# Kernel optimization log

Measured on AMD Instinct MI355X. Metric: run time of the kernel, lower is better.

## Reference

```python
import jax, jax.numpy as jnp
import numpy as np

B, S, V, D, H, L, FF = 2, 1024, 32000, 512, 8, 4, 2048
DK = D // H
WIN, GLOB = 128, 16
EPS = 1e-5


def setup_inputs() -> dict:
    key = jax.random.key(0)
    ks = jax.random.split(key, 12)
    def rn(k, shape, s=0.02):
        return jax.random.normal(k, shape, jnp.float32) * s
    ln2 = jnp.stack([jnp.ones((L, 2, D)), jnp.zeros((L, 2, D))], axis=2)   # [L, 2 norms, (scale,bias), D]
    ln3 = jnp.stack([jnp.ones((L, 3, D)), jnp.zeros((L, 3, D))], axis=2)   # [L, 3 norms, (scale,bias), D]
    fln = jnp.stack([jnp.ones((D,)), jnp.zeros((D,))], axis=0)             # [(scale,bias), D]
    return {
        "src": jax.random.randint(ks[0], (B, S), 0, V),
        "tgt": jax.random.randint(ks[1], (B, S), 0, V),
        "enc_embed": rn(ks[2], (V, D)),
        "dec_embed": rn(ks[3], (V, D)),
        "enc_attn_w": rn(ks[4], (L, 4, D, D)),   # q,k,v,o projections
        "enc_attn_b": jnp.zeros((L, 4, D)),
        "enc_ln": ln2,
        "enc_ffn_w1": rn(ks[5], (L, D, FF)),
        "enc_ffn_b1": jnp.zeros((L, FF)),
        "enc_ffn_w2": rn(ks[6], (L, FF, D)),
        "enc_ffn_b2": jnp.zeros((L, D)),
        "enc_final_ln": fln,
        "dec_attn_w": rn(ks[7], (L, 8, D, D)),   # self q,k,v,o then cross q,k,v,o
        "dec_attn_b": jnp.zeros((L, 8, D)),
        "dec_ln": ln3,
        "dec_ffn_w1": rn(ks[8], (L, D, FF)),
        "dec_ffn_b1": jnp.zeros((L, FF)),
        "dec_ffn_w2": rn(ks[9], (L, FF, D)),
        "dec_ffn_b2": jnp.zeros((L, D)),
        "dec_final_ln": fln,
        "out_w": rn(ks[10], (D, V)),
        "out_b": jnp.zeros((V,)),
    }


def _ln(x, p):
    m = jnp.mean(x, -1, keepdims=True)
    v = jnp.var(x, -1, keepdims=True)
    return p[0] * (x - m) * jax.lax.rsqrt(v + EPS) + p[1]


def _rope(x):
    # x: [B, H, S, DK]; half-split rotary embedding
    half = DK // 2
    pos = jnp.arange(x.shape[2], dtype=jnp.float32)
    inv = 1.0 / (10000.0 ** (jnp.arange(half, dtype=jnp.float32) / half))
    ang = pos[:, None] * inv[None, :]                   # [S, half]
    c, s = jnp.cos(ang), jnp.sin(ang)
    x1, x2 = x[..., :half], x[..., half:]
    return jnp.concatenate([x1 * c - x2 * s, x1 * s + x2 * c], axis=-1)


def _mask(n, causal):
    # local sliding window + global tokens, optional causal
    i = jnp.arange(n)[:, None]
    j = jnp.arange(n)[None, :]
    allowed = jnp.abs(i - j) <= WIN
    allowed = allowed | (i < GLOB) | (j < GLOB)
    if causal:
        allowed = allowed & (j <= i)
    return allowed


def _attn(q_in, k_in, v_in, w, b, causal):
    # w: [4, D, D] (q,k,v,o), b: [4, D]
    def heads(x, idx):
        y = x @ w[idx] + b[idx]
        return y.reshape(x.shape[0], x.shape[1], H, DK).transpose(0, 2, 1, 3)  # [B,H,S,DK]
    Q, K, Vh = heads(q_in, 0), heads(k_in, 1), heads(v_in, 2)
    Q, K = _rope(Q), _rope(K)
    scores = jnp.einsum('bhqd,bhkd->bhqk', Q, K) / np.sqrt(DK).astype(np.float32)
    scores = jnp.where(_mask(q_in.shape[1], causal)[None, None], scores, -1e9)
    A = jax.nn.softmax(scores, axis=-1)
    o = jnp.einsum('bhqk,bhkd->bhqd', A, Vh).transpose(0, 2, 1, 3).reshape(q_in.shape[0], q_in.shape[1], D)
    return o @ w[3] + b[3]


def _ffn(x, w1, b1, w2, b2):
    return jax.nn.gelu(x @ w1 + b1) @ w2 + b2


def _forward(src, tgt, enc_embed, dec_embed, enc_attn_w, enc_attn_b, enc_ln,
             enc_ffn_w1, enc_ffn_b1, enc_ffn_w2, enc_ffn_b2, enc_final_ln,
             dec_attn_w, dec_attn_b, dec_ln, dec_ffn_w1, dec_ffn_b1,
             dec_ffn_w2, dec_ffn_b2, dec_final_ln, out_w, out_b):
    sqrt_d = np.sqrt(D).astype(np.float32)
    # encoder
    x = enc_embed[src] * sqrt_d
    for l in range(L):
        n = _ln(x, enc_ln[l, 0])
        x = x + _attn(n, n, n, enc_attn_w[l], enc_attn_b[l], False)
        n = _ln(x, enc_ln[l, 1])
        x = x + _ffn(n, enc_ffn_w1[l], enc_ffn_b1[l], enc_ffn_w2[l], enc_ffn_b2[l])
    mem = _ln(x, enc_final_ln)
    # decoder
    y = dec_embed[tgt] * sqrt_d
    for l in range(L):
        n = _ln(y, dec_ln[l, 0])
        y = y + _attn(n, n, n, dec_attn_w[l, :4], dec_attn_b[l, :4], True)
        n = _ln(y, dec_ln[l, 1])
        y = y + _attn(n, mem, mem, dec_attn_w[l, 4:], dec_attn_b[l, 4:], False)
        n = _ln(y, dec_ln[l, 2])
        y = y + _ffn(n, dec_ffn_w1[l], dec_ffn_b1[l], dec_ffn_w2[l], dec_ffn_b2[l])
    y = _ln(y, dec_final_ln)
    return y @ out_w + out_b


def reference(src, tgt, enc_embed, dec_embed, enc_attn_w, enc_attn_b, enc_ln,
              enc_ffn_w1, enc_ffn_b1, enc_ffn_w2, enc_ffn_b2, enc_final_ln,
              dec_attn_w, dec_attn_b, dec_ln, dec_ffn_w1, dec_ffn_b1,
              dec_ffn_w2, dec_ffn_b2, dec_final_ln, out_w, out_b):
    return _forward(src, tgt, enc_embed, dec_embed, enc_attn_w, enc_attn_b, enc_ln,
                    enc_ffn_w1, enc_ffn_b1, enc_ffn_w2, enc_ffn_b2, enc_final_ln,
                    dec_attn_w, dec_attn_b, dec_ln, dec_ffn_w1, dec_ffn_b1,
                    dec_ffn_w2, dec_ffn_b2, dec_final_ln, out_w, out_b)
```

## Files before the change

kernel.cpp:

```cpp
#include <hip/hip_runtime.h>
#include <cstdint>
#include <cstddef>

#define S_LEN 1024
#define DM 512
#define NHEAD 8
#define HDIM 64
#define NLAYER 4
#define FFD 2048
#define VOC 32000
#define WINSZ 128
#define GLOBSZ 16

using half8 = __attribute__((ext_vector_type(8))) _Float16;
using f32x4 = __attribute__((ext_vector_type(4))) float;

static __device__ __forceinline__ f32x4 mfma16(half8 a, half8 b, f32x4 c) {
  return __builtin_amdgcn_mfma_f32_16x16x32_f16(a, b, c, 0, 0, 0);
}

typedef __attribute__((address_space(1))) const void gvoid;
typedef __attribute__((address_space(3))) void lvoid;
static __device__ __forceinline__ void gload16(const void* g, void* l) {
  __builtin_amdgcn_global_load_lds((gvoid*)g, (lvoid*)l, 16, 0, 0);
}
template <int N>
static __device__ __forceinline__ void waitv() {
  asm volatile("s_waitcnt vmcnt(%0)" :: "i"(N) : "memory");
}

__global__ __launch_bounds__(256) void transpose2_k(const float* __restrict__ inA,
                                                    const float* __restrict__ inB,
                                                    _Float16* __restrict__ outA,
                                                    _Float16* __restrict__ outB,
                                                    int R, int C, int splitZ)
{
  __shared__ float t[32][33];
  int z = blockIdx.z;
  const float* ip;
  _Float16* op;
  if (z < splitZ) { ip = inA + (size_t)z * R * C; op = outA + (size_t)z * R * C; }
  else { ip = inB + (size_t)(z - splitZ) * R * C; op = outB + (size_t)(z - splitZ) * R * C; }
  int c0 = blockIdx.x * 32, r0 = blockIdx.y * 32;
  int tx = threadIdx.x & 31, ty = threadIdx.x >> 5;
#pragma unroll
  for (int i = 0; i < 32; i += 8)
    t[ty + i][tx] = ip[(size_t)(r0 + ty + i) * C + c0 + tx];
  __syncthreads();
#pragma unroll
  for (int i = 0; i < 32; i += 8)
    op[(size_t)(c0 + ty + i) * R + r0 + tx] = (_Float16)t[tx][ty + i];
}

__global__ __launch_bounds__(256) void embed2_k(const int* __restrict__ src,
                                                const int* __restrict__ tgt,
                                                const float* __restrict__ enc_embed,
                                                const float* __restrict__ dec_embed,
                                                const float* __restrict__ enc_ln0,
                                                const float* __restrict__ dec_ln0,
                                                float* __restrict__ xbuf,
                                                float* __restrict__ ybuf,
                                                _Float16* __restrict__ nbuf,
                                                _Float16* __restrict__ nbuf2)
{
  int which = blockIdx.y;
  const int* ids = which ? tgt : src;
  const float* emb = which ? dec_embed : enc_embed;
  const float* gamma = which ? dec_ln0 : enc_ln0;
  const float* beta = gamma + 512;
  float* xout = which ? ybuf : xbuf;
  _Float16* nout = which ? nbuf2 : nbuf;

  int row = blockIdx.x * 4 + (threadIdx.x >> 6);
  int lane = threadIdx.x & 63;
  const float* er = emb + (size_t)ids[row] * DM + lane * 8;
  float4 v0 = *(const float4*)er;
  float4 v1 = *(const float4*)(er + 4);
  float vals[8] = {v0.x, v0.y, v0.z, v0.w, v1.x, v1.y, v1.z, v1.w};
  float s = 0.f, ss = 0.f;
#pragma unroll
  for (int j = 0; j < 8; ++j) {
    vals[j] *= 22.627416997969522f;
    s += vals[j]; ss += vals[j] * vals[j];
  }
#pragma unroll
  for (int m = 1; m < 64; m <<= 1) { s += __shfl_xor(s, m); ss += __shfl_xor(ss, m); }
  float mean = s * (1.f / 512.f);
  float var = ss * (1.f / 512.f) - mean * mean;
  float rstd = rsqrtf(var + 1e-5f);
  float* xr = xout + (size_t)row * DM + lane * 8;
  _Float16* orow = nout + (size_t)row * DM + lane * 8;
  const float* gp = gamma + lane * 8;
  const float* bp = beta + lane * 8;
#pragma unroll
  for (int j = 0; j < 8; ++j) {
    xr[j] = vals[j];
    orow[j] = (_Float16)(gp[j] * (vals[j] - mean) * rstd + bp[j]);
  }
}

__global__ __launch_bounds__(256) void ln_k(const float* __restrict__ x,
                                            const float* __restrict__ gamma,
                                            const float* __restrict__ beta,
                                            _Float16* __restrict__ outp)
{
  int row = blockIdx.x * 4 + (threadIdx.x >> 6);
  int lane = threadIdx.x & 63;
  const float* xr = x + (size_t)row * DM + lane * 8;
  float4 v0 = *(const float4*)xr;
  float4 v1 = *(const float4*)(xr + 4);
  float vals[8] = {v0.x, v0.y, v0.z, v0.w, v1.x, v1.y, v1.z, v1.w};
  float s = 0.f, ss = 0.f;
#pragma unroll
  for (int j = 0; j < 8; ++j) { s += vals[j]; ss += vals[j] * vals[j]; }
#pragma unroll
  for (int m = 1; m < 64; m <<= 1) { s += __shfl_xor(s, m); ss += __shfl_xor(ss, m); }
  float mean = s * (1.f / 512.f);
  float var = ss * (1.f / 512.f) - mean * mean;
  float rstd = rsqrtf(var + 1e-5f);
  _Float16* orow = outp + (size_t)row * DM + lane * 8;
  const float* gp = gamma + lane * 8;
  const float* bp = beta + lane * 8;
#pragma unroll
  for (int j = 0; j < 8; ++j)
    orow[j] = (_Float16)(gp[j] * (vals[j] - mean) * rstd + bp[j]);
}

template <int BM, int BN, int EPI, int MODE, bool SWZ = false, bool NT = false>
__global__ __launch_bounds__(256) void gemm_k(const _Float16* __restrict__ A,
                                              const _Float16* __restrict__ B,
                                              const float* __restrict__ bias,
                                              const float* __restrict__ resid,
                                              void* __restrict__ Cout,
                                              _Float16* __restrict__ vtout,
                                              int M, int N, int K)
{
  constexpr bool WIDE = (BN >= 64);
  constexpr int WAVE_M = WIDE ? BM / 4 : BM / 2;
  constexpr int WAVE_N = WIDE ? BN : BN / 2;
  constexpr int FMW = WAVE_M / 16;
  constexpr int FNW = WIDE ? BN / 16 : BN / 32;
  constexpr int LPS = BM / 32 + BN / 32;
  static_assert(MODE == 0 || (WIDE && BN == 64), "rope modes need 64-col waves");

  __shared__ __align__(16) _Float16 As[3][BM * 64];
  __shared__ __align__(16) _Float16 Bs[3][BN * 64];
  const int tid = threadIdx.x;
  const int lane = tid & 63, wid = tid >> 6;
  const int g = lane >> 4, ql = lane & 15;

  int bm, bn;
  if constexpr (SWZ) {
    const int gx = gridDim.x;
    const int nwg = gx * gridDim.y;
    const int orig = blockIdx.y * gx + blockIdx.x;
    const int q = nwg >> 3, r = nwg & 7;
    const int xcd = orig & 7, rest = orig >> 3;
    const int id = (xcd < r ? xcd * (q + 1) : r * (q + 1) + (xcd - r) * q) + rest;
    bm = (id % gx) * BM; bn = (id / gx) * BN;
  } else {
    bm = blockIdx.x * BM; bn = blockIdx.y * BN;
  }
  const int wm = WIDE ? wid * WAVE_M : (wid >> 1) * WAVE_M;
  const int wn = WIDE ? 0 : (wid & 1) * WAVE_N;

  const _Float16* Bp;
  if constexpr (MODE == 2) {
    int srcrow0 = ((bn >> 10) * 8 + 5 + ((bn >> 9) & 1)) * 512 + (bn & 511);
    Bp = B + (size_t)srcrow0 * K;
  } else {
    Bp = B + (size_t)bn * K;
  }

  f32x4 acc[FMW][FNW];
#pragma unroll
  for (int a = 0; a < FMW; ++a)
#pragma unroll
    for (int b = 0; b < FNW; ++b) acc[a][b] = f32x4{0.f, 0.f, 0.f, 0.f};

  auto stage = [&](int buf, int kt) {
#pragma unroll
    for (int r2 = 0; r2 < BM / 32; ++r2) {
      int off = r2 * 4096 + tid * 16;
      int row = off >> 7, slot = (off >> 4) & 7;
      gload16(A + (size_t)(bm + row) * K + kt + ((slot ^ (row & 7)) << 3),
              (char*)&As[buf][0] + r2 * 4096 + wid * 1024);
    }
#pragma unroll
    for (int r2 = 0; r2 < BN / 32; ++r2) {
      int off = r2 * 4096 + tid * 16;
      int row = off >> 7, slot = (off >> 4) & 7;
      gload16(Bp + (size_t)row * K + kt + ((slot ^ (row & 7)) << 3),
              (char*)&Bs[buf][0] + r2 * 4096 + wid * 1024);
    }
  };

  auto compute = [&](int cur) {
#pragma unroll
    for (int kk = 0; kk < 2; ++kk) {
      half8 af[FMW], bf[FNW];
#pragma unroll
      for (int a = 0; a < FMW; ++a) {
        int row = wm + a * 16 + ql;
        af[a] = *(const half8*)((const char*)&As[cur][0] + row * 128 + (((kk * 4 + g) ^ (row & 7)) << 4));
      }
#pragma unroll
      for (int b = 0; b < FNW; ++b) {
        int row = wn + b * 16 + ql;
        bf[b] = *(const half8*)((const char*)&Bs[cur][0] + row * 128 + (((kk * 4 + g) ^ (row & 7)) << 4));
      }
#pragma unroll
      for (int a = 0; a < FMW; ++a)
#pragma unroll
        for (int b = 0; b < FNW; ++b) acc[a][b] = mfma16(af[a], bf[b], acc[a][b]);
    }
  };

  const int nk = K >> 6;
  stage(0, 0);
  stage(1, 64);
  for (int t = 0; t < nk; ++t) {
    if (t + 1 < nk) waitv<LPS>(); else waitv<0>();
    __builtin_amdgcn_s_barrier();
    __builtin_amdgcn_sched_barrier(0);
    compute(t % 3);
    if (t + 2 < nk) stage((t + 2) % 3, (t + 2) << 6);
  }

#pragma unroll
  for (int a = 0; a < FMW; ++a) {
    const int row0 = bm + wm + a * 16 + g * 4;
    float v[FNW][4];
#pragma unroll
    for (int b2 = 0; b2 < FNW; ++b2) {
      int col = bn + wn + b2 * 16 + ql;
      float bv;
      if constexpr (MODE == 2) {
        int bcol = ((col >> 10) * 8 + 5 + ((col >> 9) & 1)) * 512 + (col & 511);
        bv = bias[bcol];
      } else {
        bv = bias[col];
      }
#pragma unroll
      for (int r2 = 0; r2 < 4; ++r2) v[b2][r2] = acc[a][b2][r2] + bv;
    }
    if constexpr (MODE != 0) {
      const int seg = bn >> 9;
      bool dorope = (MODE == 3) || (MODE == 1 && seg < 2) ||
                    (MODE == 2 && ((bn >> 9) & 1) == 0);
      if (dorope) {
        const float scale = (MODE == 3 || (MODE == 1 && seg == 0)) ? 0.125f : 1.0f;
#pragma unroll
        for (int b2 = 0; b2 < 2; ++b2) {
          int d = b2 * 16 + ql;
          float inv = __expf(-(float)d * 0.28782313662425574f);
#pragma unroll
          for (int r2 = 0; r2 < 4; ++r2) {
            float sp = (float)((row0 & 1023) + r2);
            float sn, cs; __sincosf(sp * inv, &sn, &cs);
            float x1 = v[b2][r2], x2 = v[b2 + 2][r2];
            v[b2][r2]     = (x1 * cs - x2 * sn) * scale;
            v[b2 + 2][r2] = (x1 * sn + x2 * cs) * scale;
          }
        }
      }
    }
#pragma unroll
    for (int b2 = 0; b2 < FNW; ++b2) {
      int col = bn + wn + b2 * 16 + ql;
      if constexpr (MODE == 1) {
        if (col < 1024) {
#pragma unroll
          for (int r2 = 0; r2 < 4; ++r2)
            ((_Float16*)Cout)[(size_t)(row0 + r2) * 1024 + col] = (_Float16)v[b2][r2];
        } else {
          int rowidx = ((row0 >> 10) << 9) + (col - 1024);
          union { _Float16 h[4]; uint2 u; } pk;
#pragma unroll
          for (int r2 = 0; r2 < 4; ++r2) pk.h[r2] = (_Float16)v[b2][r2];
          *(uint2*)&vtout[((size_t)rowidx << 10) + (row0 & 1023)] = pk.u;
        }
      } else if constexpr (MODE == 2) {
        if ((col & 1023) < 512) {
#pragma unroll
          for (int r2 = 0; r2 < 4; ++r2)
            ((_Float16*)Cout)[(size_t)(row0 + r2) * 2048 + ((col >> 10) << 9) + (col & 511)] = (_Float16)v[b2][r2];
        } else {
          int rowidx = (col & ~1023) + ((row0 >> 10) << 9) + (col & 511);
          union { _Float16 h[4]; uint2 u; } pk;
#pragma unroll
          for (int r2 = 0; r2 < 4; ++r2) pk.h[r2] = (_Float16)v[b2][r2];
          *(uint2*)&vtout[((size_t)rowidx << 10) + (row0 & 1023)] = pk.u;
        }
      } else {
#pragma unroll
        for (int r2 = 0; r2 < 4; ++r2) {
          float x = v[b2][r2];
          if constexpr (EPI == 1) {
            float u = x;
            x = u / (1.f + __expf(-1.5957691216057308f * (u + 0.044715f * u * u * u)));
          }
          if constexpr (EPI == 2) x += resid[(size_t)(row0 + r2) * N + col];
          if constexpr (EPI == 0 || EPI == 1)
            ((_Float16*)Cout)[(size_t)(row0 + r2) * N + col] = (_Float16)x;
          else if constexpr (NT)
            __builtin_nontemporal_store(x, &((float*)Cout)[(size_t)(row0 + r2) * N + col]);
          else
            ((float*)Cout)[(size_t)(row0 + r2) * N + col] = x;
        }
      }
    }
  }
}

template <bool CAUSAL>
__global__ __launch_bounds__(128) void attn_k(const _Float16* __restrict__ qb, int qs, int qoff,
                                              const _Float16* __restrict__ kb, int ks, int koff,
                                              const _Float16* __restrict__ vt,
                                              _Float16* __restrict__ out)
{
  __shared__ _Float16 plds[2][16 * 40];
  const int bh = blockIdx.y, b = bh >> 3, h = bh & 7;
  const int wid = threadIdx.x >> 6, lane = threadIdx.x & 63;
  const int g = lane >> 4, ql = lane & 15;
  const int q0 = blockIdx.x * 32 + wid * 16;
  const size_t rb = (size_t)b * S_LEN;

  half8 qf0, qf1;
  {
    const _Float16* qp = qb + (rb + q0 + ql) * qs + qoff + h * HDIM + g * 8;
    qf0 = *(const half8*)qp;
    qf1 = *(const half8*)(qp + 32);
  }
  float mrun[4] = {-1e30f, -1e30f, -1e30f, -1e30f};
  float srun[4] = {0.f, 0.f, 0.f, 0.f};
  f32x4 oacc[4];
#pragma unroll
  for (int c = 0; c < 4; ++c) oacc[c] = f32x4{0.f, 0.f, 0.f, 0.f};

  const _Float16* vbase = vt + (((size_t)(b * 512 + h * HDIM)) << 10);
  _Float16* pw = plds[wid];

  auto proc = [&](int k0) {
    const _Float16* kp = kb + (rb + k0 + ql) * ks + koff + h * HDIM + g * 8;
    half8 kf00 = *(const half8*)kp;
    half8 kf01 = *(const half8*)(kp + 32);
    half8 kf10 = *(const half8*)(kp + (size_t)16 * ks);
    half8 kf11 = *(const half8*)(kp + (size_t)16 * ks + 32);

    f32x4 s0 = f32x4{0.f, 0.f, 0.f, 0.f};
    f32x4 s1 = f32x4{0.f, 0.f, 0.f, 0.f};
    s0 = mfma16(qf0, kf00, s0); s0 = mfma16(qf1, kf01, s0);
    s1 = mfma16(qf0, kf10, s1); s1 = mfma16(qf1, kf11, s1);

    float p0[4], p1[4];
#pragma unroll
    for (int r = 0; r < 4; ++r) {
      int i = q0 + 4 * g + r;
      int j0 = k0 + ql, j1 = j0 + 16;
      float a0 = s0[r], a1 = s1[r];
      int d0 = i - j0, d1 = i - j1;
      bool ok0 = (d0 <= WINSZ && d0 >= -WINSZ) || (i < GLOBSZ) || (j0 < GLOBSZ);
      bool ok1 = (d1 <= WINSZ && d1 >= -WINSZ) || (i < GLOBSZ) || (j1 < GLOBSZ);
      if (CAUSAL) { ok0 = ok0 && (j0 <= i); ok1 = ok1 && (j1 <= i); }
      a0 = ok0 ? a0 : -1e9f;
      a1 = ok1 ? a1 : -1e9f;
      float mx = fmaxf(a0, a1);
      mx = fmaxf(mx, __shfl_xor(mx, 1));
      mx = fmaxf(mx, __shfl_xor(mx, 2));
      mx = fmaxf(mx, __shfl_xor(mx, 4));
      mx = fmaxf(mx, __shfl_xor(mx, 8));
      float mnew = fmaxf(mrun[r], mx);
      float alpha = __expf(mrun[r] - mnew);
      float e0 = __expf(a0 - mnew), e1 = __expf(a1 - mnew);
      float ps = e0 + e1;
      ps += __shfl_xor(ps, 1);
      ps += __shfl_xor(ps, 2);
      ps += __shfl_xor(ps, 4);
      ps += __shfl_xor(ps, 8);
      srun[r] = srun[r] * alpha + ps;
      mrun[r] = mnew;
#pragma unroll
      for (int c = 0; c < 4; ++c) oacc[c][r] *= alpha;
      p0[r] = e0; p1[r] = e1;
    }
#pragma unroll
    for (int r = 0; r < 4; ++r) {
      pw[(4 * g + r) * 40 + ql] = (_Float16)p0[r];
      pw[(4 * g + r) * 40 + 16 + ql] = (_Float16)p1[r];
    }
    half8 pa = *(const half8*)&pw[ql * 40 + g * 8];
#pragma unroll
    for (int c = 0; c < 4; ++c) {
      half8 vf = *(const half8*)(vbase + (((size_t)(16 * c + ql)) << 10) + k0 + 8 * g);
      oacc[c] = mfma16(pa, vf, oacc[c]);
    }
  };

  const int kend = CAUSAL ? (q0 + 16) : S_LEN;
  int lo = 0, hi = kend;
  if (q0 >= GLOBSZ) {
    lo = (q0 - WINSZ) & ~31;
    if (lo < 0) lo = 0;
    if (!CAUSAL) {
      int h2 = q0 + 16 + WINSZ;
      hi = (h2 < kend) ? h2 : kend;
    }
  }
  if (lo > 0) proc(0);
  for (int k0 = lo; k0 < hi; k0 += 32) proc(k0);

#pragma unroll
  for (int c = 0; c < 4; ++c)
#pragma unroll
    for (int r = 0; r < 4; ++r) {
      float val = oacc[c][r] / srun[r];
      out[(rb + q0 + 4 * g + r) * DM + h * HDIM + 16 * c + ql] = (_Float16)val;
    }
}

extern "C" void kernel_launch(void* const* d_in, const int* in_sizes, int n_in,
                              void* d_out, int out_size, void* d_ws, size_t ws_size,
                              hipStream_t stream)
{
  const int*   src         = (const int*)d_in[0];
  const int*   tgt         = (const int*)d_in[1];
  const float* enc_embed   = (const float*)d_in[2];
  const float* dec_embed   = (const float*)d_in[3];
  const float* enc_attn_w  = (const float*)d_in[4];
  const float* enc_attn_b  = (const float*)d_in[5];
  const float* enc_ln      = (const float*)d_in[6];
  const float* enc_ffn_w1  = (const float*)d_in[7];
  const float* enc_ffn_b1  = (const float*)d_in[8];
  const float* enc_ffn_w2  = (const float*)d_in[9];
  const float* enc_ffn_b2  = (const float*)d_in[10];
  const float* enc_fln     = (const float*)d_in[11];
  const float* dec_attn_w  = (const float*)d_in[12];
  const float* dec_attn_b  = (const float*)d_in[13];
  const float* dec_ln      = (const float*)d_in[14];
  const float* dec_ffn_w1  = (const float*)d_in[15];
  const float* dec_ffn_b1  = (const float*)d_in[16];
  const float* dec_ffn_w2  = (const float*)d_in[17];
  const float* dec_ffn_b2  = (const float*)d_in[18];
  const float* dec_fln     = (const float*)d_in[19];
  const float* out_w       = (const float*)d_in[20];
  const float* out_b       = (const float*)d_in[21];
  float* logits = (float*)d_out;

  char* wsp = (char*)d_ws;
  size_t off = 0;
  auto alloc = [&](size_t bytes) -> void* {
    void* p = wsp + off;
    off += (bytes + 255) & ~(size_t)255;
    return p;
  };
  _Float16* enc_attn_wt = (_Float16*)alloc((size_t)16 * 512 * 512 * 2);
  _Float16* dec_attn_wt = (_Float16*)alloc((size_t)32 * 512 * 512 * 2);
  _Float16* e_ffn1_wt   = (_Float16*)alloc((size_t)4 * 2048 * 512 * 2);
  _Float16* e_ffn2_wt   = (_Float16*)alloc((size_t)4 * 2048 * 512 * 2);
  _Float16* d_ffn1_wt   = (_Float16*)alloc((size_t)4 * 2048 * 512 * 2);
  _Float16* d_ffn2_wt   = (_Float16*)alloc((size_t)4 * 2048 * 512 * 2);
  _Float16* out_wt      = (_Float16*)alloc((size_t)VOC * 512 * 2);
  float*    xbuf        = (float*)alloc((size_t)2048 * 512 * 4);
  float*    ybuf        = (float*)alloc((size_t)2048 * 512 * 4);
  _Float16* nbuf        = (_Float16*)alloc((size_t)2048 * 512 * 2);
  _Float16* nbuf2       = (_Float16*)alloc((size_t)2048 * 512 * 2);
  _Float16* qkvb        = (_Float16*)alloc((size_t)2048 * 1024 * 2);
  _Float16* aob         = (_Float16*)alloc((size_t)2048 * 512 * 2);
  _Float16* hbuf        = (_Float16*)alloc((size_t)2048 * 2048 * 2);
  _Float16* memb        = (_Float16*)alloc((size_t)2048 * 512 * 2);
  _Float16* cqb         = (_Float16*)alloc((size_t)2048 * 512 * 2);
  _Float16* ckvb        = (_Float16*)alloc((size_t)2048 * 2048 * 2);
  _Float16* vts         = (_Float16*)alloc((size_t)2 * 512 * 1024 * 2);
  _Float16* vtc         = (_Float16*)alloc((size_t)8 * 512 * 1024 * 2);

  transpose2_k<<<dim3(16, 16, 48), 256, 0, stream>>>(enc_attn_w, dec_attn_w,
                                                     enc_attn_wt, dec_attn_wt, 512, 512, 16);
  transpose2_k<<<dim3(64, 16, 8), 256, 0, stream>>>(enc_ffn_w1, dec_ffn_w1,
                                                    e_ffn1_wt, d_ffn1_wt, 512, 2048, 4);
  transpose2_k<<<dim3(16, 64, 8), 256, 0, stream>>>(enc_ffn_w2, dec_ffn_w2,
                                                    e_ffn2_wt, d_ffn2_wt, 2048, 512, 4);
  transpose2_k<<<dim3(1000, 16, 1), 256, 0, stream>>>(out_w, out_w, out_wt, out_wt, 512, VOC, 1);

  embed2_k<<<dim3(512, 2), 256, 0, stream>>>(src, tgt, enc_embed, dec_embed,
                                             enc_ln, dec_ln, xbuf, ybuf, nbuf, nbuf2);

  for (int l = 0; l < NLAYER; ++l) {
    const float* g0 = enc_ln + ((size_t)(l * 2 + 0) * 2 + 0) * 512;
    if (l > 0) ln_k<<<512, 256, 0, stream>>>(xbuf, g0, g0 + 512, nbuf);
    gemm_k<64, 64, 0, 1><<<dim3(32, 24), 256, 0, stream>>>(
        nbuf, enc_attn_wt + (size_t)l * 4 * 262144,
        enc_attn_b + (size_t)l * 4 * 512, nullptr, qkvb, vts, 2048, 1536, 512);
    attn_k<false><<<dim3(32, 16), 128, 0, stream>>>(qkvb, 1024, 0, qkvb, 1024, 512, vts, aob);
    gemm_k<64, 32, 2, 0><<<dim3(32, 16), 256, 0, stream>>>(
        aob, enc_attn_wt + (size_t)(l * 4 + 3) * 262144,
        enc_attn_b + (size_t)(l * 4 + 3) * 512, xbuf, xbuf, nullptr, 2048, 512, 512);
    const float* g1 = enc_ln + ((size_t)(l * 2 + 1) * 2 + 0) * 512;
    ln_k<<<512, 256, 0, stream>>>(xbuf, g1, g1 + 512, nbuf);
    gemm_k<64, 64, 1, 0><<<dim3(32, 32), 256, 0, stream>>>(
        nbuf, e_ffn1_wt + (size_t)l * 2048 * 512,
        enc_ffn_b1 + (size_t)l * 2048, nullptr, hbuf, nullptr, 2048, 2048, 512);
    gemm_k<64, 32, 2, 0><<<dim3(32, 16), 256, 0, stream>>>(
        hbuf, e_ffn2_wt + (size_t)l * 512 * 2048,
        enc_ffn_b2 + (size_t)l * 512, xbuf, xbuf, nullptr, 2048, 512, 2048);
  }
  ln_k<<<512, 256, 0, stream>>>(xbuf, enc_fln, enc_fln + 512, memb);

  gemm_k<64, 64, 0, 2><<<dim3(32, 64), 256, 0, stream>>>(
      memb, dec_attn_wt, dec_attn_b, nullptr, ckvb, vtc, 2048, 4096, 512);

  for (int l = 0; l < NLAYER; ++l) {
    const float* g0 = dec_ln + ((size_t)(l * 3 + 0) * 2 + 0) * 512;
    const _Float16* dn = (l == 0) ? nbuf2 : nbuf;
    if (l > 0) ln_k<<<512, 256, 0, stream>>>(ybuf, g0, g0 + 512, nbuf);
    gemm_k<64, 64, 0, 1><<<dim3(32, 24), 256, 0, stream>>>(
        dn, dec_attn_wt + (size_t)l * 8 * 262144,
        dec_attn_b + (size_t)l * 8 * 512, nullptr, qkvb, vts, 2048, 1536, 512);
    attn_k<true><<<dim3(32, 16), 128, 0, stream>>>(qkvb, 1024, 0, qkvb, 1024, 512, vts, aob);
    gemm_k<64, 32, 2, 0><<<dim3(32, 16), 256, 0, stream>>>(
        aob, dec_attn_wt + (size_t)(l * 8 + 3) * 262144,
        dec_attn_b + (size_t)(l * 8 + 3) * 512, ybuf, ybuf, nullptr, 2048, 512, 512);
    const float* g1 = dec_ln + ((size_t)(l * 3 + 1) * 2 + 0) * 512;
    ln_k<<<512, 256, 0, stream>>>(ybuf, g1, g1 + 512, nbuf);
    gemm_k<64, 64, 0, 3><<<dim3(32, 8), 256, 0, stream>>>(
        nbuf, dec_attn_wt + (size_t)(l * 8 + 4) * 262144,
        dec_attn_b + (size_t)(l * 8 + 4) * 512, nullptr, cqb, nullptr, 2048, 512, 512);
    attn_k<false><<<dim3(32, 16), 128, 0, stream>>>(cqb, 512, 0, ckvb, 2048, l * 512,
                                                    vtc + ((size_t)l << 20), aob);
    gemm_k<64, 32, 2, 0><<<dim3(32, 16), 256, 0, stream>>>(
        aob, dec_attn_wt + (size_t)(l * 8 + 7) * 262144,
        dec_attn_b + (size_t)(l * 8 + 7) * 512, ybuf, ybuf, nullptr, 2048, 512, 512);
    const float* g2 = dec_ln + ((size_t)(l * 3 + 2) * 2 + 0) * 512;
    ln_k<<<512, 256, 0, stream>>>(ybuf, g2, g2 + 512, nbuf);
    gemm_k<64, 64, 1, 0><<<dim3(32, 32), 256, 0, stream>>>(
        nbuf, d_ffn1_wt + (size_t)l * 2048 * 512,
        dec_ffn_b1 + (size_t)l * 2048, nullptr, hbuf, nullptr, 2048, 2048, 512);
    gemm_k<64, 32, 2, 0><<<dim3(32, 16), 256, 0, stream>>>(
        hbuf, d_ffn2_wt + (size_t)l * 512 * 2048,
        dec_ffn_b2 + (size_t)l * 512, ybuf, ybuf, nullptr, 2048, 512, 2048);
  }

  ln_k<<<512, 256, 0, stream>>>(ybuf, dec_fln, dec_fln + 512, nbuf);
  gemm_k<128, 64, 3, 0, true, true><<<dim3(16, 500), 256, 0, stream>>>(
      nbuf, out_wt, out_b, nullptr, logits, nullptr, 2048, VOC, 512);
}
```

Baseline: 976.0 us.

## Fuse LayerNorm into the following GEMM prologue with full-K A tile in LDS

Adds a gemmln_k kernel that reads fp32 residual rows, computes LayerNorm per row, and writes the normalized fp16 row for the whole K=512 into LDS. It then streams B tiles double-buffered to do the projection with the existing RoPE, V-transpose and GELU epilogues. All standalone ln_k launches before QKV, cross-Q, cross-KV and FFN1 GEMMs are removed, and embed no longer normalizes. This drops the fp16 round trip and the extra launches, but each column block recomputes LayerNorm for its 64 rows. The 64KB A tile in LDS may also limit occupancy.

```diff
diff --git a/kernel.cpp b/kernel.cpp
--- a/kernel.cpp
+++ b/kernel.cpp
@@ -56,47 +56,23 @@
                                                 const int* __restrict__ tgt,
                                                 const float* __restrict__ enc_embed,
                                                 const float* __restrict__ dec_embed,
-                                                const float* __restrict__ enc_ln0,
-                                                const float* __restrict__ dec_ln0,
                                                 float* __restrict__ xbuf,
-                                                float* __restrict__ ybuf,
-                                                _Float16* __restrict__ nbuf,
-                                                _Float16* __restrict__ nbuf2)
+                                                float* __restrict__ ybuf)
 {
   int which = blockIdx.y;
   const int* ids = which ? tgt : src;
   const float* emb = which ? dec_embed : enc_embed;
-  const float* gamma = which ? dec_ln0 : enc_ln0;
-  const float* beta = gamma + 512;
   float* xout = which ? ybuf : xbuf;
-  _Float16* nout = which ? nbuf2 : nbuf;
 
   int row = blockIdx.x * 4 + (threadIdx.x >> 6);
   int lane = threadIdx.x & 63;
   const float* er = emb + (size_t)ids[row] * DM + lane * 8;
   float4 v0 = *(const float4*)er;
   float4 v1 = *(const float4*)(er + 4);
-  float vals[8] = {v0.x, v0.y, v0.z, v0.w, v1.x, v1.y, v1.z, v1.w};
-  float s = 0.f, ss = 0.f;
-#pragma unroll
-  for (int j = 0; j < 8; ++j) {
-    vals[j] *= 22.627416997969522f;
-    s += vals[j]; ss += vals[j] * vals[j];
-  }
-#pragma unroll
-  for (int m = 1; m < 64; m <<= 1) { s += __shfl_xor(s, m); ss += __shfl_xor(ss, m); }
-  float mean = s * (1.f / 512.f);
-  float var = ss * (1.f / 512.f) - mean * mean;
-  float rstd = rsqrtf(var + 1e-5f);
   float* xr = xout + (size_t)row * DM + lane * 8;
-  _Float16* orow = nout + (size_t)row * DM + lane * 8;
-  const float* gp = gamma + lane * 8;
-  const float* bp = beta + lane * 8;
-#pragma unroll
-  for (int j = 0; j < 8; ++j) {
-    xr[j] = vals[j];
-    orow[j] = (_Float16)(gp[j] * (vals[j] - mean) * rstd + bp[j]);
-  }
+  const float sc = 22.627416997969522f;
+  xr[0] = v0.x * sc; xr[1] = v0.y * sc; xr[2] = v0.z * sc; xr[3] = v0.w * sc;
+  xr[4] = v1.x * sc; xr[5] = v1.y * sc; xr[6] = v1.z * sc; xr[7] = v1.w * sc;
 }
 
 __global__ __launch_bounds__(256) void ln_k(const float* __restrict__ x,
@@ -124,6 +100,191 @@
 #pragma unroll
   for (int j = 0; j < 8; ++j)
     orow[j] = (_Float16)(gp[j] * (vals[j] - mean) * rstd + bp[j]);
+}
+
+template <int EPI, int MODE>
+__global__ __launch_bounds__(256) void gemmln_k(const float* __restrict__ A,
+                                                const _Float16* __restrict__ B,
+                                                const float* __restrict__ gamma,
+                                                const float* __restrict__ beta,
+                                                const float* __restrict__ bias,
+                                                void* __restrict__ Cout,
+                                                _Float16* __restrict__ vtout,
+                                                int N)
+{
+  constexpr int FNW = 4;
+  __shared__ __align__(16) _Float16 As[64 * 512];
+  __shared__ __align__(16) _Float16 Bs[2][64 * 64];
+  const int tid = threadIdx.x;
+  const int lane = tid & 63, wid = tid >> 6;
+  const int g = lane >> 4, ql = lane & 15;
+  const int bm = blockIdx.x * 64, bn = blockIdx.y * 64;
+
+  const _Float16* Bp;
+  if constexpr (MODE == 2) {
+    int srcrow0 = ((bn >> 10) * 8 + 5 + ((bn >> 9) & 1)) * 512 + (bn & 511);
+    Bp = B + (size_t)srcrow0 * 512;
+  } else {
+    Bp = B + (size_t)bn * 512;
+  }
+
+  auto stageB = [&](int buf, int kt) {
+#pragma unroll
+    for (int r2 = 0; r2 < 2; ++r2) {
+      int off = r2 * 4096 + tid * 16;
+      int row = off >> 7, slot = (off >> 4) & 7;
+      gload16(Bp + (size_t)row * 512 + kt + ((slot ^ (row & 7)) << 3),
+              (char*)&Bs[buf][0] + r2 * 4096 + wid * 1024);
+    }
+  };
+
+  stageB(0, 0);
+
+  {
+    const int row = wid * 16 + (lane >> 2);
+    const int chunk = lane & 3;
+    const float* ap = A + (size_t)(bm + row) * 512 + chunk * 128;
+    float s = 0.f, ss = 0.f;
+#pragma unroll
+    for (int j = 0; j < 32; ++j) {
+      float4 v = *(const float4*)(ap + j * 4);
+      s += v.x + v.y + v.z + v.w;
+      ss += v.x * v.x + v.y * v.y + v.z * v.z + v.w * v.w;
+    }
+    s += __shfl_xor(s, 1); ss += __shfl_xor(ss, 1);
+    s += __shfl_xor(s, 2); ss += __shfl_xor(ss, 2);
+    const float mean = s * (1.f / 512.f);
+    const float rstd = rsqrtf(ss * (1.f / 512.f) - mean * mean + 1e-5f);
+    const float* gp = gamma + chunk * 128;
+    const float* bp = beta + chunk * 128;
+    auto nrm = [&](float a, float gg, float bb) {
+      return (_Float16)(gg * (a - mean) * rstd + bb);
+    };
+#pragma unroll
+    for (int j = 0; j < 16; ++j) {
+      float4 a0 = *(const float4*)(ap + j * 8);
+      float4 a1 = *(const float4*)(ap + j * 8 + 4);
+      float4 g0 = *(const float4*)(gp + j * 8);
+      float4 g1 = *(const float4*)(gp + j * 8 + 4);
+      float4 b0 = *(const float4*)(bp + j * 8);
+      float4 b1 = *(const float4*)(bp + j * 8 + 4);
+      union { _Float16 h[8]; uint4 u; } pk;
+      pk.h[0] = nrm(a0.x, g0.x, b0.x); pk.h[1] = nrm(a0.y, g0.y, b0.y);
+      pk.h[2] = nrm(a0.z, g0.z, b0.z); pk.h[3] = nrm(a0.w, g0.w, b0.w);
+      pk.h[4] = nrm(a1.x, g1.x, b1.x); pk.h[5] = nrm(a1.y, g1.y, b1.y);
+      pk.h[6] = nrm(a1.z, g1.z, b1.z); pk.h[7] = nrm(a1.w, g1.w, b1.w);
+      int slot16 = chunk * 16 + j;
+      int seg = slot16 >> 3, sub = slot16 & 7;
+      *(uint4*)((char*)As + row * 1024 + seg * 128 + ((sub ^ (row & 7)) << 4)) = pk.u;
+    }
+  }
+  asm volatile("s_waitcnt lgkmcnt(0)" ::: "memory");
+
+  f32x4 acc[FNW];
+#pragma unroll
+  for (int b = 0; b < FNW; ++b) acc[b] = f32x4{0.f, 0.f, 0.f, 0.f};
+
+  const int arow = wid * 16 + ql;
+  const int abyte_base = arow * 1024;
+
+#pragma unroll
+  for (int t = 0; t < 8; ++t) {
+    __builtin_amdgcn_s_barrier();
+    if (t + 1 < 8) stageB((t + 1) & 1, (t + 1) << 6);
+    if (t + 1 < 8) waitv<2>(); else waitv<0>();
+    __builtin_amdgcn_sched_barrier(0);
+    const int cur = t & 1;
+#pragma unroll
+    for (int kk = 0; kk < 2; ++kk) {
+      half8 af = *(const half8*)((const char*)As + abyte_base + t * 128 +
+                                 (((kk * 4 + g) ^ (arow & 7)) << 4));
+      half8 bf[FNW];
+#pragma unroll
+      for (int b = 0; b < FNW; ++b) {
+        int row = b * 16 + ql;
+        bf[b] = *(const half8*)((const char*)&Bs[cur][0] + row * 128 +
+                                (((kk * 4 + g) ^ (row & 7)) << 4));
+      }
+#pragma unroll
+      for (int b = 0; b < FNW; ++b) acc[b] = mfma16(af, bf[b], acc[b]);
+    }
+  }
+
+  const int row0 = bm + wid * 16 + g * 4;
+  float v[FNW][4];
+#pragma unroll
+  for (int b2 = 0; b2 < FNW; ++b2) {
+    int col = bn + b2 * 16 + ql;
+    float bv;
+    if constexpr (MODE == 2) {
+      int bcol = ((col >> 10) * 8 + 5 + ((col >> 9) & 1)) * 512 + (col & 511);
+      bv = bias[bcol];
+    } else {
+      bv = bias[col];
+    }
+#pragma unroll
+    for (int r2 = 0; r2 < 4; ++r2) v[b2][r2] = acc[b2][r2] + bv;
+  }
+  if constexpr (MODE != 0) {
+    const int seg = bn >> 9;
+    bool dorope = (MODE == 3) || (MODE == 1 && seg < 2) ||
+                  (MODE == 2 && ((bn >> 9) & 1) == 0);
+    if (dorope) {
+      const float scale = (MODE == 3 || (MODE == 1 && seg == 0)) ? 0.125f : 1.0f;
+#pragma unroll
+      for (int b2 = 0; b2 < 2; ++b2) {
+        int d = b2 * 16 + ql;
+        float inv = __expf(-(float)d * 0.28782313662425574f);
+#pragma unroll
+        for (int r2 = 0; r2 < 4; ++r2) {
+          float sp = (float)((row0 & 1023) + r2);
+          float sn, cs; __sincosf(sp * inv, &sn, &cs);
+          float x1 = v[b2][r2], x2 = v[b2 + 2][r2];
+          v[b2][r2]     = (x1 * cs - x2 * sn) * scale;
+          v[b2 + 2][r2] = (x1 * sn + x2 * cs) * scale;
+        }
+      }
+    }
+  }
+#pragma unroll
+  for (int b2 = 0; b2 < FNW; ++b2) {
+    int col = bn + b2 * 16 + ql;
+    if constexpr (MODE == 1) {
+      if (col < 1024) {
+#pragma unroll
+        for (int r2 = 0; r2 < 4; ++r2)
+          ((_Float16*)Cout)[(size_t)(row0 + r2) * 1024 + col] = (_Float16)v[b2][r2];
+      } else {
+        int rowidx = ((row0 >> 10) << 9) + (col - 1024);
+        union { _Float16 h[4]; uint2 u; } pk;
+#pragma unroll
+        for (int r2 = 0; r2 < 4; ++r2) pk.h[r2] = (_Float16)v[b2][r2];
+        *(uint2*)&vtout[((size_t)rowidx << 10) + (row0 & 1023)] = pk.u;
+      }
+    } else if constexpr (MODE == 2) {
+      if ((col & 1023) < 512) {
+#pragma unroll
+        for (int r2 = 0; r2 < 4; ++r2)
+          ((_Float16*)Cout)[(size_t)(row0 + r2) * 2048 + ((col >> 10) << 9) + (col & 511)] = (_Float16)v[b2][r2];
+      } else {
+        int rowidx = (col & ~1023) + ((row0 >> 10) << 9) + (col & 511);
+        union { _Float16 h[4]; uint2 u; } pk;
+#pragma unroll
+        for (int r2 = 0; r2 < 4; ++r2) pk.h[r2] = (_Float16)v[b2][r2];
+        *(uint2*)&vtout[((size_t)rowidx << 10) + (row0 & 1023)] = pk.u;
+      }
+    } else {
+#pragma unroll
+      for (int r2 = 0; r2 < 4; ++r2) {
+        float x = v[b2][r2];
+        if constexpr (EPI == 1) {
+          float u = x;
+          x = u / (1.f + __expf(-1.5957691216057308f * (u + 0.044715f * u * u * u)));
+        }
+        ((_Float16*)Cout)[(size_t)(row0 + r2) * N + col] = (_Float16)x;
+      }
+    }
+  }
 }
 
 template <int BM, int BN, int EPI, int MODE, bool SWZ = false, bool NT = false>
@@ -141,7 +302,6 @@
   constexpr int FMW = WAVE_M / 16;
   constexpr int FNW = WIDE ? BN / 16 : BN / 32;
   constexpr int LPS = BM / 32 + BN / 32;
-  static_assert(MODE == 0 || (WIDE && BN == 64), "rope modes need 64-col waves");
 
   __shared__ __align__(16) _Float16 As[3][BM * 64];
   __shared__ __align__(16) _Float16 Bs[3][BN * 64];
@@ -164,13 +324,7 @@
   const int wm = WIDE ? wid * WAVE_M : (wid >> 1) * WAVE_M;
   const int wn = WIDE ? 0 : (wid & 1) * WAVE_N;
 
-  const _Float16* Bp;
-  if constexpr (MODE == 2) {
-    int srcrow0 = ((bn >> 10) * 8 + 5 + ((bn >> 9) & 1)) * 512 + (bn & 511);
-    Bp = B + (size_t)srcrow0 * K;
-  } else {
-    Bp = B + (size_t)bn * K;
-  }
+  const _Float16* Bp = B + (size_t)bn * K;
 
   f32x4 acc[FMW][FNW];
 #pragma unroll
@@ -230,84 +384,24 @@
 #pragma unroll
   for (int a = 0; a < FMW; ++a) {
     const int row0 = bm + wm + a * 16 + g * 4;
-    float v[FNW][4];
 #pragma unroll
     for (int b2 = 0; b2 < FNW; ++b2) {
       int col = bn + wn + b2 * 16 + ql;
-      float bv;
-      if constexpr (MODE == 2) {
-        int bcol = ((col >> 10) * 8 + 5 + ((col >> 9) & 1)) * 512 + (col & 511);
-        bv = bias[bcol];
-      } else {
-        bv = bias[col];
-      }
-#pragma unroll
-      for (int r2 = 0; r2 < 4; ++r2) v[b2][r2] = acc[a][b2][r2] + bv;
-    }
-    if constexpr (MODE != 0) {
-      const int seg = bn >> 9;
-      bool dorope = (MODE == 3) || (MODE == 1 && seg < 2) ||
-                    (MODE == 2 && ((bn >> 9) & 1) == 0);
-      if (dorope) {
-        const float scale = (MODE == 3 || (MODE == 1 && seg == 0)) ? 0.125f : 1.0f;
-#pragma unroll
-        for (int b2 = 0; b2 < 2; ++b2) {
-          int d = b2 * 16 + ql;
-          float inv = __expf(-(float)d * 0.28782313662425574f);
-#pragma unroll
-          for (int r2 = 0; r2 < 4; ++r2) {
-            float sp = (float)((row0 & 1023) + r2);
-            float sn, cs; __sincosf(sp * inv, &sn, &cs);
-            float x1 = v[b2][r2], x2 = v[b2 + 2][r2];
-            v[b2][r2]     = (x1 * cs - x2 * sn) * scale;
-            v[b2 + 2][r2] = (x1 * sn + x2 * cs) * scale;
-          }
+      float bv = bias[col];
+#pragma unroll
+      for (int r2 = 0; r2 < 4; ++r2) {
+        float x = acc[a][b2][r2] + bv;
+        if constexpr (EPI == 1) {
+          float u = x;
+          x = u / (1.f + __expf(-1.5957691216057308f * (u + 0.044715f * u * u * u)));
         }
-      }
-    }
-#pragma unroll
-    for (int b2 = 0; b2 < FNW; ++b2) {
-      int col = bn + wn + b2 * 16 + ql;
-      if constexpr (MODE == 1) {
-        if (col < 1024) {
-#pragma unroll
-          for (int r2 = 0; r2 < 4; ++r2)
-            ((_Float16*)Cout)[(size_t)(row0 + r2) * 1024 + col] = (_Float16)v[b2][r2];
-        } else {
-          int rowidx = ((row0 >> 10) << 9) + (col - 1024);
-          union { _Float16 h[4]; uint2 u; } pk;
-#pragma unroll
-          for (int r2 = 0; r2 < 4; ++r2) pk.h[r2] = (_Float16)v[b2][r2];
-          *(uint2*)&vtout[((size_t)rowidx << 10) + (row0 & 1023)] = pk.u;
-        }
-      } else if constexpr (MODE == 2) {
-        if ((col & 1023) < 512) {
-#pragma unroll
-          for (int r2 = 0; r2 < 4; ++r2)
-            ((_Float16*)Cout)[(size_t)(row0 + r2) * 2048 + ((col >> 10) << 9) + (col & 511)] = (_Float16)v[b2][r2];
-        } else {
-          int rowidx = (col & ~1023) + ((row0 >> 10) << 9) + (col & 511);
-          union { _Float16 h[4]; uint2 u; } pk;
-#pragma unroll
-          for (int r2 = 0; r2 < 4; ++r2) pk.h[r2] = (_Float16)v[b2][r2];
-          *(uint2*)&vtout[((size_t)rowidx << 10) + (row0 & 1023)] = pk.u;
-        }
-      } else {
-#pragma unroll
-        for (int r2 = 0; r2 < 4; ++r2) {
-          float x = v[b2][r2];
-          if constexpr (EPI == 1) {
-            float u = x;
-            x = u / (1.f + __expf(-1.5957691216057308f * (u + 0.044715f * u * u * u)));
-          }
-          if constexpr (EPI == 2) x += resid[(size_t)(row0 + r2) * N + col];
-          if constexpr (EPI == 0 || EPI == 1)
-            ((_Float16*)Cout)[(size_t)(row0 + r2) * N + col] = (_Float16)x;
-          else if constexpr (NT)
-            __builtin_nontemporal_store(x, &((float*)Cout)[(size_t)(row0 + r2) * N + col]);
-          else
-            ((float*)Cout)[(size_t)(row0 + r2) * N + col] = x;
-        }
+        if constexpr (EPI == 2) x += resid[(size_t)(row0 + r2) * N + col];
+        if constexpr (EPI == 0 || EPI == 1)
+          ((_Float16*)Cout)[(size_t)(row0 + r2) * N + col] = (_Float16)x;
+        else if constexpr (NT)
+          __builtin_nontemporal_store(x, &((float*)Cout)[(size_t)(row0 + r2) * N + col]);
+        else
+          ((float*)Cout)[(size_t)(row0 + r2) * N + col] = x;
       }
     }
   }
@@ -464,11 +558,9 @@
   float*    xbuf        = (float*)alloc((size_t)2048 * 512 * 4);
   float*    ybuf        = (float*)alloc((size_t)2048 * 512 * 4);
   _Float16* nbuf        = (_Float16*)alloc((size_t)2048 * 512 * 2);
-  _Float16* nbuf2       = (_Float16*)alloc((size_t)2048 * 512 * 2);
   _Float16* qkvb        = (_Float16*)alloc((size_t)2048 * 1024 * 2);
   _Float16* aob         = (_Float16*)alloc((size_t)2048 * 512 * 2);
   _Float16* hbuf        = (_Float16*)alloc((size_t)2048 * 2048 * 2);
-  _Float16* memb        = (_Float16*)alloc((size_t)2048 * 512 * 2);
   _Float16* cqb         = (_Float16*)alloc((size_t)2048 * 512 * 2);
   _Float16* ckvb        = (_Float16*)alloc((size_t)2048 * 2048 * 2);
   _Float16* vts         = (_Float16*)alloc((size_t)2 * 512 * 1024 * 2);
@@ -482,59 +574,51 @@
                                                     e_ffn2_wt, d_ffn2_wt, 2048, 512, 4);
   transpose2_k<<<dim3(1000, 16, 1), 256, 0, stream>>>(out_w, out_w, out_wt, out_wt, 512, VOC, 1);
 
-  embed2_k<<<dim3(512, 2), 256, 0, stream>>>(src, tgt, enc_embed, dec_embed,
-                                             enc_ln, dec_ln, xbuf, ybuf, nbuf, nbuf2);
+  embed2_k<<<dim3(512, 2), 256, 0, stream>>>(src, tgt, enc_embed, dec_embed, xbuf, ybuf);
 
   for (int l = 0; l < NLAYER; ++l) {
     const float* g0 = enc_ln + ((size_t)(l * 2 + 0) * 2 + 0) * 512;
-    if (l > 0) ln_k<<<512, 256, 0, stream>>>(xbuf, g0, g0 + 512, nbuf);
-    gemm_k<64, 64, 0, 1><<<dim3(32, 24), 256, 0, stream>>>(
-        nbuf, enc_attn_wt + (size_t)l * 4 * 262144,
-        enc_attn_b + (size_t)l * 4 * 512, nullptr, qkvb, vts, 2048, 1536, 512);
+    gemmln_k<0, 1><<<dim3(32, 24), 256, 0, stream>>>(
+        xbuf, enc_attn_wt + (size_t)l * 4 * 262144, g0, g0 + 512,
+        enc_attn_b + (size_t)l * 4 * 512, qkvb, vts, 1536);
     attn_k<false><<<dim3(32, 16), 128, 0, stream>>>(qkvb, 1024, 0, qkvb, 1024, 512, vts, aob);
     gemm_k<64, 32, 2, 0><<<dim3(32, 16), 256, 0, stream>>>(
         aob, enc_attn_wt + (size_t)(l * 4 + 3) * 262144,
         enc_attn_b + (size_t)(l * 4 + 3) * 512, xbuf, xbuf, nullptr, 2048, 512, 512);
     const float* g1 = enc_ln + ((size_t)(l * 2 + 1) * 2 + 0) * 512;
-    ln_k<<<512, 256, 0, stream>>>(xbuf, g1, g1 + 512, nbuf);
-    gemm_k<64, 64, 1, 0><<<dim3(32, 32), 256, 0, stream>>>(
-        nbuf, e_ffn1_wt + (size_t)l * 2048 * 512,
-        enc_ffn_b1 + (size_t)l * 2048, nullptr, hbuf, nullptr, 2048, 2048, 512);
+    gemmln_k<1, 0><<<dim3(32, 32), 256, 0, stream>>>(
+        xbuf, e_ffn1_wt + (size_t)l * 2048 * 512, g1, g1 + 512,
+        enc_ffn_b1 + (size_t)l * 2048, hbuf, nullptr, 2048);
     gemm_k<64, 32, 2, 0><<<dim3(32, 16), 256, 0, stream>>>(
         hbuf, e_ffn2_wt + (size_t)l * 512 * 2048,
         enc_ffn_b2 + (size_t)l * 512, xbuf, xbuf, nullptr, 2048, 512, 2048);
   }
-  ln_k<<<512, 256, 0, stream>>>(xbuf, enc_fln, enc_fln + 512, memb);
-
-  gemm_k<64, 64, 0, 2><<<dim3(32, 64), 256, 0, stream>>>(
-      memb, dec_attn_wt, dec_attn_b, nullptr, ckvb, vtc, 2048, 4096, 512);
+
+  gemmln_k<0, 2><<<dim3(32, 64), 256, 0, stream>>>(
+      xbuf, dec_attn_wt, enc_fln, enc_fln + 512, dec_attn_b, ckvb, vtc, 4096);
 
   for (int l = 0; l < NLAYER; ++l) {
     const float* g0 = dec_ln + ((size_t)(l * 3 + 0) * 2 + 0) * 512;
-    const _Float16* dn = (l == 0) ? nbuf2 : nbuf;
-    if (l > 0) ln_k<<<512, 256, 0, stream>>>(ybuf, g0, g0 + 512, nbuf);
-    gemm_k<64, 64, 0, 1><<<dim3(32, 24), 256, 0, stream>>>(
-        dn, dec_attn_wt + (size_t)l * 8 * 262144,
-        dec_attn_b + (size_t)l * 8 * 512, nullptr, qkvb, vts, 2048, 1536, 512);
+    gemmln_k<0, 1><<<dim3(32, 24), 256, 0, stream>>>(
+        ybuf, dec_attn_wt + (size_t)l * 8 * 262144, g0, g0 + 512,
+        dec_attn_b + (size_t)l * 8 * 512, qkvb, vts, 1536);
     attn_k<true><<<dim3(32, 16), 128, 0, stream>>>(qkvb, 1024, 0, qkvb, 1024, 512, vts, aob);
     gemm_k<64, 32, 2, 0><<<dim3(32, 16), 256, 0, stream>>>(
         aob, dec_attn_wt + (size_t)(l * 8 + 3) * 262144,
         dec_attn_b + (size_t)(l * 8 + 3) * 512, ybuf, ybuf, nullptr, 2048, 512, 512);
     const float* g1 = dec_ln + ((size_t)(l * 3 + 1) * 2 + 0) * 512;
-    ln_k<<<512, 256, 0, stream>>>(ybuf, g1, g1 + 512, nbuf);
-    gemm_k<64, 64, 0, 3><<<dim3(32, 8), 256, 0, stream>>>(
-        nbuf, dec_attn_wt + (size_t)(l * 8 + 4) * 262144,
-        dec_attn_b + (size_t)(l * 8 + 4) * 512, nullptr, cqb, nullptr, 2048, 512, 512);
+    gemmln_k<0, 3><<<dim3(32, 8), 256, 0, stream>>>(
+        ybuf, dec_attn_wt + (size_t)(l * 8 + 4) * 262144, g1, g1 + 512,
+        dec_attn_b + (size_t)(l * 8 + 4) * 512, cqb, nullptr, 512);
     attn_k<false><<<dim3(32, 16), 128, 0, stream>>>(cqb, 512, 0, ckvb, 2048, l * 512,
                                                     vtc + ((size_t)l << 20), aob);
     gemm_k<64, 32, 2, 0><<<dim3(32, 16), 256, 0, stream>>>(
         aob, dec_attn_wt + (size_t)(l * 8 + 7) * 262144,
         dec_attn_b + (size_t)(l * 8 + 7) * 512, ybuf, ybuf, nullptr, 2048, 512, 512);
     const float* g2 = dec_ln + ((size_t)(l * 3 + 2) * 2 + 0) * 512;
-    ln_k<<<512, 256, 0, stream>>>(ybuf, g2, g2 + 512, nbuf);
-    gemm_k<64, 64, 1, 0><<<dim3(32, 32), 256, 0, stream>>>(
-        nbuf, d_ffn1_wt + (size_t)l * 2048 * 512,
-        dec_ffn_b1 + (size_t)l * 2048, nullptr, hbuf, nullptr, 2048, 2048, 512);
+    gemmln_k<1, 0><<<dim3(32, 32), 256, 0, stream>>>(
+        ybuf, d_ffn1_wt + (size_t)l * 2048 * 512, g2, g2 + 512,
+        dec_ffn_b1 + (size_t)l * 2048, hbuf, nullptr, 2048);
     gemm_k<64, 32, 2, 0><<<dim3(32, 16), 256, 0, stream>>>(
         hbuf, d_ffn2_wt + (size_t)l * 512 * 2048,
         dec_ffn_b2 + (size_t)l * 512, ybuf, ybuf, nullptr, 2048, 512, 2048);
```

Result: slower. 1.849 ms (+89.4%).

## Add dedicated logits GEMM kernel with XCD-aware tile remap and swizzled LDS

Applied to the files above, without the earlier changes.

Adds a specialized kernel for the final vocabulary projection. It uses 128x64 tiles, double-buffered direct global-to-LDS loads with an XOR swizzle, and a remap of block IDs so neighbouring tiles land on the same XCD for L2 reuse. Results are written with nontemporal stores. It also flips a template flag (likely the same XCD remap or a swizzle option) on several existing gemm_k launches. The goal is better cache locality and fewer LDS bank conflicts, at the cost of extra code and a dependence on what the unseen template flag means.

```diff
diff --git a/kernel.cpp b/kernel.cpp
--- a/kernel.cpp
+++ b/kernel.cpp
@@ -309,6 +309,95 @@
             ((float*)Cout)[(size_t)(row0 + r2) * N + col] = x;
         }
       }
+    }
+  }
+}
+
+__global__ __launch_bounds__(256) void gemmlg_k(const _Float16* __restrict__ A,
+                                                const _Float16* __restrict__ B,
+                                                const float* __restrict__ bias,
+                                                float* __restrict__ Cout,
+                                                int N, int K)
+{
+  __shared__ __align__(16) _Float16 As[2][128 * 64];
+  __shared__ __align__(16) _Float16 Bs[2][64 * 64];
+  const int tid = threadIdx.x;
+  const int lane = tid & 63, wid = tid >> 6;
+  const int g = lane >> 4, ql = lane & 15;
+
+  const int gx = gridDim.x;
+  const int nwg = gx * gridDim.y;
+  const int orig = blockIdx.y * gx + blockIdx.x;
+  const int q = nwg >> 3, r = nwg & 7;
+  const int xcd = orig & 7, rest = orig >> 3;
+  const int id = (xcd < r ? xcd * (q + 1) : r * (q + 1) + (xcd - r) * q) + rest;
+  const int bm = (id % gx) * 128, bn = (id / gx) * 64;
+  const int wm = wid * 32;
+
+  const _Float16* Bp = B + (size_t)bn * K;
+
+  f32x4 acc[2][4];
+#pragma unroll
+  for (int a = 0; a < 2; ++a)
+#pragma unroll
+    for (int b = 0; b < 4; ++b) acc[a][b] = f32x4{0.f, 0.f, 0.f, 0.f};
+
+  auto stage = [&](int buf, int kt) {
+#pragma unroll
+    for (int r2 = 0; r2 < 4; ++r2) {
+      int off = r2 * 4096 + tid * 16;
+      int row = off >> 7, slot = (off >> 4) & 7;
+      gload16(A + (size_t)(bm + row) * K + kt + ((slot ^ (row & 7)) << 3),
+              (char*)&As[buf][0] + r2 * 4096 + wid * 1024);
+    }
+#pragma unroll
+    for (int r2 = 0; r2 < 2; ++r2) {
+      int off = r2 * 4096 + tid * 16;
+      int row = off >> 7, slot = (off >> 4) & 7;
+      gload16(Bp + (size_t)row * K + kt + ((slot ^ (row & 7)) << 3),
+              (char*)&Bs[buf][0] + r2 * 4096 + wid * 1024);
+    }
+  };
+
+  const int nk = K >> 6;
+  stage(0, 0);
+  for (int t = 0; t < nk; ++t) {
+    waitv<0>();
+    __builtin_amdgcn_s_barrier();
+    __builtin_amdgcn_sched_barrier(0);
+    if (t + 1 < nk) stage((t + 1) & 1, (t + 1) << 6);
+    const int cur = t & 1;
+#pragma unroll
+    for (int kk = 0; kk < 2; ++kk) {
+      half8 af[2], bf[4];
+#pragma unroll
+      for (int a = 0; a < 2; ++a) {
+        int row = wm + a * 16 + ql;
+        af[a] = *(const half8*)((const char*)&As[cur][0] + row * 128 + (((kk * 4 + g) ^ (row & 7)) << 4));
+      }
+#pragma unroll
+      for (int b = 0; b < 4; ++b) {
+        int row = b * 16 + ql;
+        bf[b] = *(const half8*)((const char*)&Bs[cur][0] + row * 128 + (((kk * 4 + g) ^ (row & 7)) << 4));
+      }
+#pragma unroll
+      for (int a = 0; a < 2; ++a)
+#pragma unroll
+        for (int b = 0; b < 4; ++b) acc[a][b] = mfma16(af[a], bf[b], acc[a][b]);
+    }
+  }
+
+#pragma unroll
+  for (int a = 0; a < 2; ++a) {
+    const int row0 = bm + wm + a * 16 + g * 4;
+#pragma unroll
+    for (int b2 = 0; b2 < 4; ++b2) {
+      int col = bn + b2 * 16 + ql;
+      float bv = bias[col];
+#pragma unroll
+      for (int r2 = 0; r2 < 4; ++r2)
+        __builtin_nontemporal_store(acc[a][b2][r2] + bv,
+                                    &Cout[(size_t)(row0 + r2) * N + col]);
     }
   }
 }
@@ -488,7 +577,7 @@
   for (int l = 0; l < NLAYER; ++l) {
     const float* g0 = enc_ln + ((size_t)(l * 2 + 0) * 2 + 0) * 512;
     if (l > 0) ln_k<<<512, 256, 0, stream>>>(xbuf, g0, g0 + 512, nbuf);
-    gemm_k<64, 64, 0, 1><<<dim3(32, 24), 256, 0, stream>>>(
+    gemm_k<64, 64, 0, 1, true><<<dim3(32, 24), 256, 0, stream>>>(
         nbuf, enc_attn_wt + (size_t)l * 4 * 262144,
         enc_attn_b + (size_t)l * 4 * 512, nullptr, qkvb, vts, 2048, 1536, 512);
     attn_k<false><<<dim3(32, 16), 128, 0, stream>>>(qkvb, 1024, 0, qkvb, 1024, 512, vts, aob);
@@ -497,7 +586,7 @@
         enc_attn_b + (size_t)(l * 4 + 3) * 512, xbuf, xbuf, nullptr, 2048, 512, 512);
     const float* g1 = enc_ln + ((size_t)(l * 2 + 1) * 2 + 0) * 512;
     ln_k<<<512, 256, 0, stream>>>(xbuf, g1, g1 + 512, nbuf);
-    gemm_k<64, 64, 1, 0><<<dim3(32, 32), 256, 0, stream>>>(
+    gemm_k<64, 64, 1, 0, true><<<dim3(32, 32), 256, 0, stream>>>(
         nbuf, e_ffn1_wt + (size_t)l * 2048 * 512,
         enc_ffn_b1 + (size_t)l * 2048, nullptr, hbuf, nullptr, 2048, 2048, 512);
     gemm_k<64, 32, 2, 0><<<dim3(32, 16), 256, 0, stream>>>(
@@ -506,14 +595,14 @@
   }
   ln_k<<<512, 256, 0, stream>>>(xbuf, enc_fln, enc_fln + 512, memb);
 
-  gemm_k<64, 64, 0, 2><<<dim3(32, 64), 256, 0, stream>>>(
+  gemm_k<64, 64, 0, 2, true><<<dim3(32, 64), 256, 0, stream>>>(
       memb, dec_attn_wt, dec_attn_b, nullptr, ckvb, vtc, 2048, 4096, 512);
 
   for (int l = 0; l < NLAYER; ++l) {
     const float* g0 = dec_ln + ((size_t)(l * 3 + 0) * 2 + 0) * 512;
     const _Float16* dn = (l == 0) ? nbuf2 : nbuf;
     if (l > 0) ln_k<<<512, 256, 0, stream>>>(ybuf, g0, g0 + 512, nbuf);
-    gemm_k<64, 64, 0, 1><<<dim3(32, 24), 256, 0, stream>>>(
+    gemm_k<64, 64, 0, 1, true><<<dim3(32, 24), 256, 0, stream>>>(
         dn, dec_attn_wt + (size_t)l * 8 * 262144,
         dec_attn_b + (size_t)l * 8 * 512, nullptr, qkvb, vts, 2048, 1536, 512);
     attn_k<true><<<dim3(32, 16), 128, 0, stream>>>(qkvb, 1024, 0, qkvb, 1024, 512, vts, aob);
@@ -532,7 +621,7 @@
         dec_attn_b + (size_t)(l * 8 + 7) * 512, ybuf, ybuf, nullptr, 2048, 512, 512);
     const float* g2 = dec_ln + ((size_t)(l * 3 + 2) * 2 + 0) * 512;
     ln_k<<<512, 256, 0, stream>>>(ybuf, g2, g2 + 512, nbuf);
-    gemm_k<64, 64, 1, 0><<<dim3(32, 32), 256, 0, stream>>>(
+    gemm_k<64, 64, 1, 0, true><<<dim3(32, 32), 256, 0, stream>>>(
         nbuf, d_ffn1_wt + (size_t)l * 2048 * 512,
         dec_ffn_b1 + (size_t)l * 2048, nullptr, hbuf, nullptr, 2048, 2048, 512);
     gemm_k<64, 32, 2, 0><<<dim3(32, 16), 256, 0, stream>>>(
@@ -541,6 +630,5 @@
   }
 
   ln_k<<<512, 256, 0, stream>>>(ybuf, dec_fln, dec_fln + 512, nbuf);
-  gemm_k<128, 64, 3, 0, true, true><<<dim3(16, 500), 256, 0, stream>>>(
-      nbuf, out_wt, out_b, nullptr, logits, nullptr, 2048, VOC, 512);
-}
+  gemmlg_k<<<dim3(16, 500), 256, 0, stream>>>(nbuf, out_wt, out_b, logits, VOC, 512);
+}
```

Result: no change. 967.1 us (median of 2 runs) (-0.9%).
